# Kernel tuning notes

Hardware: AMD Instinct MI355X
Metric: run time of the kernel (lower is better)

The kernel has to match this reference:

```python
import jax, jax.numpy as jnp
import numpy as np

B, N_VAR, N_CLAUSE, K = 256, 10000, 40000, 3
N_NODE = N_VAR + N_CLAUSE


def setup_inputs() -> dict:
    key = jax.random.key(0)
    k1, k2, k3 = jax.random.split(key, 3)
    out = jax.random.normal(k1, (B, N_NODE), dtype=jnp.float32)
    # binary labels (torch y are 0/1 floats)
    y = (jax.random.uniform(k2, (B, N_NODE)) > 0.5).astype(jnp.float32)
    # mask: 0 on variable nodes, 1 on clause nodes
    mask = jnp.concatenate(
        [jnp.zeros((B, N_VAR), jnp.float32), jnp.ones((B, N_CLAUSE), jnp.float32)],
        axis=1,
    )
    # clauses: per graph, n_clause clauses of K variable indices in [0, n_var)
    clauses = jax.random.randint(k3, (B, N_CLAUSE, K), 0, N_VAR, dtype=jnp.int32)
    return {
        "out": out,
        "y": y,
        "mask": mask,
        "clauses": clauses,
        "n_var": N_VAR,
        "n_clause": N_CLAUSE,
    }


def _bce_with_logits(x, t):
    # elementwise BCE-with-logits: softplus(x) - x*t (numerically stable)
    return jax.nn.softplus(x) - x * t


def reference(out, y, mask, clauses, n_var, n_clause):
    b = out.shape[0]
    # loss 1: mean BCE over masked logits, divided by n_clause (per graph)
    loss1 = jnp.mean(_bce_with_logits(out * mask, y), axis=1) / n_clause  # [B]

    # hard predictions (detached in torch): sigmoid > 0.5, keep clause nodes only
    pred = (jax.nn.sigmoid(jax.lax.stop_gradient(out)) > 0.5).astype(out.dtype) * mask
    clause_active = pred[:, n_var:]  # [B, n_clause]

    # loadUnsatVariables: for each active clause, set its variables to 1.
    # Order-independent -> scatter-max of clause activation onto variable slots.
    flat_idx = (jnp.arange(b, dtype=jnp.int32)[:, None, None] * n_var
                + clauses).reshape(-1)  # [B*n_clause*K]
    vals = jnp.broadcast_to(clause_active[:, :, None], clauses.shape).reshape(-1)
    var_target = (jnp.zeros(b * n_var, out.dtype)
                  .at[flat_idx].max(vals)
                  .reshape(b, n_var))
    # target * (1 - mask): variable positions keep scatter result, clause part -> 0
    target = jnp.concatenate(
        [var_target, jnp.zeros((b, clause_active.shape[1]), out.dtype)], axis=1)

    loss2 = jnp.mean(_bce_with_logits(out * (1.0 - mask), target), axis=1) * 2.0
    return jnp.sum(loss1 + loss2)
```

## Files before the change

### kernel.cpp

```cpp
#include <hip/hip_runtime.h>

#define BB      256
#define NVAR    10000
#define NCLAUSE 40000
#define NNODE   50000
#define NT      1024
#define NV4C    (NCLAUSE / 4)
#define NV4V    (NVAR / 4)
#define LDSW    2504


__device__ __forceinline__ float softplusf(float x) {
    return fmaxf(x, 0.f) + __logf(1.f + __expf(-fabsf(x)));
}

__device__ __forceinline__ float bce4(const float4 q, const unsigned f) {
    float s = 0.f;
    s += softplusf(q.x) - q.x * (float)( f        & 1u);
    s += softplusf(q.y) - q.y * (float)((f >> 8)  & 1u);
    s += softplusf(q.z) - q.z * (float)((f >> 16) & 1u);
    s += softplusf(q.w) - q.w * (float)((f >> 24) & 1u);
    return s;
}

__global__ __launch_bounds__(NT) void k_all(const float* __restrict__ outp,
                                            const float* __restrict__ yp,
                                            const int*   __restrict__ cl,
                                            float* __restrict__ accum,
                                            unsigned* __restrict__ counter,
                                            float* __restrict__ res) {
    __shared__ unsigned fw[LDSW];
    __shared__ float red[NT / 64];
    const int b = blockIdx.x;
    const int tid = threadIdx.x;
    unsigned char* flags = (unsigned char*)fw;

    for (int i = tid; i < LDSW; i += NT) fw[i] = 0u;
    __syncthreads();

    const float4* vrow4 = (const float4*)(outp + (size_t)b * NNODE);
    const bool h1 = (tid + NT     < NV4V);
    const bool h2 = (tid + 2 * NT < NV4V);
    float4 q0, q1, q2;
    q0 = vrow4[tid];
    if (h1) q1 = vrow4[tid + NT];
    if (h2) q2 = vrow4[tid + 2 * NT];

    const float* orow = outp + (size_t)b * NNODE + NVAR;
    const float* yrow = yp   + (size_t)b * NNODE + NVAR;
    const int*   crow = cl   + (size_t)b * NCLAUSE * 3;

    float s1 = 0.f;
    for (int t = tid; t < NV4C; t += NT) {
        const float4 o4 = *(const float4*)(orow + 4 * t);
        const float4 y4 = *(const float4*)(yrow + 4 * t);
        const int4* cp = (const int4*)(crow + 12 * t);
        const int4 c0 = cp[0], c1 = cp[1], c2 = cp[2];

        s1 += softplusf(o4.x) - o4.x * y4.x;
        s1 += softplusf(o4.y) - o4.y * y4.y;
        s1 += softplusf(o4.z) - o4.z * y4.z;
        s1 += softplusf(o4.w) - o4.w * y4.w;

        if (o4.x > 0.f) { flags[c0.x] = 1; flags[c0.y] = 1; flags[c0.z] = 1; }
        if (o4.y > 0.f) { flags[c0.w] = 1; flags[c1.x] = 1; flags[c1.y] = 1; }
        if (o4.z > 0.f) { flags[c1.z] = 1; flags[c1.w] = 1; flags[c2.x] = 1; }
        if (o4.w > 0.f) { flags[c2.y] = 1; flags[c2.z] = 1; flags[c2.w] = 1; }
    }
    __syncthreads();

    float s2 = bce4(q0, fw[tid]);
    if (h1) s2 += bce4(q1, fw[tid + NT]);
    if (h2) s2 += bce4(q2, fw[tid + 2 * NT]);

    float v = s1 * (1.0f / ((float)NNODE * (float)NCLAUSE)) + s2 * (2.0f / (float)NNODE);
    #pragma unroll
    for (int off = 32; off; off >>= 1) v += __shfl_down(v, off, 64);
    const int lane = tid & 63, w = tid >> 6;
    if (lane == 0) red[w] = v;
    __syncthreads();
    if (tid == 0) {
        float r = 0.f;
        #pragma unroll
        for (int i = 0; i < NT / 64; ++i) r += red[i];
        atomicAdd(accum, r);
        __threadfence();
        const unsigned old = atomicAdd(counter, 1u);
        if (old == BB - 1) {
            const float S = atomicAdd(accum, 0.0f);
            const double ln2 = 0.6931471805599453;
            double rr = (double)S
                      + ((double)BB * NVAR * ln2) / ((double)NNODE * (double)NCLAUSE)
                      + 2.0 * ((double)BB * NCLAUSE * ln2) / (double)NNODE;
            res[0] = (float)rr;
        }
    }
}

extern "C" void kernel_launch(void* const* d_in, const int* in_sizes, int n_in,
                              void* d_out, int out_size, void* d_ws, size_t ws_size,
                              hipStream_t stream) {
    const float* outp = (const float*)d_in[0];
    const float* yp   = (const float*)d_in[1];
    const int* cl     = (const int*)d_in[3];

    float* accum = (float*)d_ws;
    unsigned* counter = (unsigned*)((char*)d_ws + 8);
    hipMemsetAsync(d_ws, 0, 16, stream);

    k_all<<<BB, NT, 0, stream>>>(outp, yp, cl, accum, counter, (float*)d_out);
}
```

Baseline: 45.78 us.

## Split each batch row across two blocks with global bitmask merge and spin barrier

Each batch row's clause work is now split across two workgroups, giving 512 blocks instead of 256 to better fill the GPU's compute units. Each block packs its LDS byte flags into a bitmask, ORs it into a global per-row buffer, and spin-waits on a per-row counter until both halves arrive. It then reads the combined mask to compute the variable-node loss on its half of the variables. This adds a larger workspace memset, global atomics, and an inter-block spin barrier, which can deadlock if the paired blocks are not co-resident.

```diff
diff --git a/kernel.cpp b/kernel.cpp
--- a/kernel.cpp
+++ b/kernel.cpp
@@ -5,53 +5,48 @@
 #define NCLAUSE 40000
 #define NNODE   50000
 #define NT      1024
-#define NV4C    (NCLAUSE / 4)
+#define NSPLIT  2
+#define CL_H    (NCLAUSE / NSPLIT)
+#define V4C_H   (CL_H / 4)
 #define NV4V    (NVAR / 4)
+#define V4V_H   (NV4V / NSPLIT)
 #define LDSW    2504
+#define NWORDS  313
+#define ROWSTR  320
 
+#define WS_ROWCNT 1024
+#define WS_BITS   2048
+#define WS_ZERO   (WS_BITS + BB * ROWSTR * 4)
 
 __device__ __forceinline__ float softplusf(float x) {
     return fmaxf(x, 0.f) + __logf(1.f + __expf(-fabsf(x)));
-}
-
-__device__ __forceinline__ float bce4(const float4 q, const unsigned f) {
-    float s = 0.f;
-    s += softplusf(q.x) - q.x * (float)( f        & 1u);
-    s += softplusf(q.y) - q.y * (float)((f >> 8)  & 1u);
-    s += softplusf(q.z) - q.z * (float)((f >> 16) & 1u);
-    s += softplusf(q.w) - q.w * (float)((f >> 24) & 1u);
-    return s;
 }
 
 __global__ __launch_bounds__(NT) void k_all(const float* __restrict__ outp,
                                             const float* __restrict__ yp,
                                             const int*   __restrict__ cl,
                                             float* __restrict__ accum,
-                                            unsigned* __restrict__ counter,
+                                            unsigned* __restrict__ fincnt,
+                                            unsigned* __restrict__ rowcnt,
+                                            unsigned* __restrict__ bits,
                                             float* __restrict__ res) {
     __shared__ unsigned fw[LDSW];
+    __shared__ unsigned comb[NWORDS];
     __shared__ float red[NT / 64];
-    const int b = blockIdx.x;
+    const int h = blockIdx.x;
+    const int b = blockIdx.y;
     const int tid = threadIdx.x;
     unsigned char* flags = (unsigned char*)fw;
 
     for (int i = tid; i < LDSW; i += NT) fw[i] = 0u;
     __syncthreads();
 
-    const float4* vrow4 = (const float4*)(outp + (size_t)b * NNODE);
-    const bool h1 = (tid + NT     < NV4V);
-    const bool h2 = (tid + 2 * NT < NV4V);
-    float4 q0, q1, q2;
-    q0 = vrow4[tid];
-    if (h1) q1 = vrow4[tid + NT];
-    if (h2) q2 = vrow4[tid + 2 * NT];
-
-    const float* orow = outp + (size_t)b * NNODE + NVAR;
-    const float* yrow = yp   + (size_t)b * NNODE + NVAR;
-    const int*   crow = cl   + (size_t)b * NCLAUSE * 3;
+    const float* orow = outp + (size_t)b * NNODE + NVAR + h * CL_H;
+    const float* yrow = yp   + (size_t)b * NNODE + NVAR + h * CL_H;
+    const int*   crow = cl   + (size_t)b * NCLAUSE * 3 + (size_t)h * CL_H * 3;
 
     float s1 = 0.f;
-    for (int t = tid; t < NV4C; t += NT) {
+    for (int t = tid; t < V4C_H; t += NT) {
         const float4 o4 = *(const float4*)(orow + 4 * t);
         const float4 y4 = *(const float4*)(yrow + 4 * t);
         const int4* cp = (const int4*)(crow + 12 * t);
@@ -69,9 +64,41 @@
     }
     __syncthreads();
 
-    float s2 = bce4(q0, fw[tid]);
-    if (h1) s2 += bce4(q1, fw[tid + NT]);
-    if (h2) s2 += bce4(q2, fw[tid + 2 * NT]);
+    unsigned* rowb = bits + (size_t)b * ROWSTR;
+    if (tid < NWORDS) {
+        unsigned r = 0;
+        #pragma unroll
+        for (int k = 0; k < 8; ++k) {
+            const unsigned u = fw[tid * 8 + k];
+            const unsigned nib = (u | (u >> 7) | (u >> 14) | (u >> 21)) & 0xFu;
+            r |= nib << (4 * k);
+        }
+        if (r) atomicOr(rowb + tid, r);
+    }
+    __syncthreads();
+    if (tid == 0) {
+        __threadfence();
+        atomicAdd(rowcnt + b, 1u);
+        while (atomicAdd(rowcnt + b, 0u) < NSPLIT) __builtin_amdgcn_s_sleep(1);
+    }
+    __syncthreads();
+
+    if (tid < NWORDS) comb[tid] = atomicOr(rowb + tid, 0u);
+    __syncthreads();
+
+    float s2 = 0.f;
+    {
+        const float* vrow = outp + (size_t)b * NNODE + h * (NVAR / NSPLIT);
+        for (int t = tid; t < V4V_H; t += NT) {
+            const int vt = h * V4V_H + t;
+            const float4 q4 = *(const float4*)(vrow + 4 * t);
+            const unsigned g = (comb[vt >> 3] >> ((4 * vt) & 31)) & 0xFu;
+            s2 += softplusf(q4.x) - q4.x * (float)( g       & 1u);
+            s2 += softplusf(q4.y) - q4.y * (float)((g >> 1) & 1u);
+            s2 += softplusf(q4.z) - q4.z * (float)((g >> 2) & 1u);
+            s2 += softplusf(q4.w) - q4.w * (float)((g >> 3) & 1u);
+        }
+    }
 
     float v = s1 * (1.0f / ((float)NNODE * (float)NCLAUSE)) + s2 * (2.0f / (float)NNODE);
     #pragma unroll
@@ -85,8 +112,8 @@
         for (int i = 0; i < NT / 64; ++i) r += red[i];
         atomicAdd(accum, r);
         __threadfence();
-        const unsigned old = atomicAdd(counter, 1u);
-        if (old == BB - 1) {
+        const unsigned old = atomicAdd(fincnt, 1u);
+        if (old == BB * NSPLIT - 1) {
             const float S = atomicAdd(accum, 0.0f);
             const double ln2 = 0.6931471805599453;
             double rr = (double)S
@@ -104,9 +131,12 @@
     const float* yp   = (const float*)d_in[1];
     const int* cl     = (const int*)d_in[3];
 
-    float* accum = (float*)d_ws;
-    unsigned* counter = (unsigned*)((char*)d_ws + 8);
-    hipMemsetAsync(d_ws, 0, 16, stream);
+    float*    accum  = (float*)d_ws;
+    unsigned* fincnt = (unsigned*)((char*)d_ws + 4);
+    unsigned* rowcnt = (unsigned*)((char*)d_ws + WS_ROWCNT);
+    unsigned* bits   = (unsigned*)((char*)d_ws + WS_BITS);
+    hipMemsetAsync(d_ws, 0, WS_ZERO, stream);
 
-    k_all<<<BB, NT, 0, stream>>>(outp, yp, cl, accum, counter, (float*)d_out);
+    dim3 grid(NSPLIT, BB);
+    k_all<<<grid, NT, 0, stream>>>(outp, yp, cl, accum, fincnt, rowcnt, bits, (float*)d_out);
 }
```

After: 72.32 us. 1.58x slower.
